# Kernel optimization log

Hardware: AMD Instinct MI355X
Metric: run time of the kernel (lower is better)

## Reference

```python
import jax, jax.numpy as jnp
import numpy as np

B, T, C = 4, 4096, 1024
NEG_INF = -1e38


def setup_inputs() -> dict:
    key = jax.random.key(0)
    ks = jax.random.split(key, 5)
    scale = 0.02  # realistic init scale for CxC projections
    x = jax.random.normal(ks[0], (B, T, C), dtype=jnp.float32)
    key_w = jax.random.normal(ks[1], (C, C), dtype=jnp.float32) * scale
    value_w = jax.random.normal(ks[2], (C, C), dtype=jnp.float32) * scale
    receptance_w = jax.random.normal(ks[3], (C, C), dtype=jnp.float32) * scale
    output_w = jax.random.normal(ks[4], (C, C), dtype=jnp.float32) * scale
    # deterministic param init matching the module's __init__
    time_decay = -5.0 + 8.0 * (jnp.arange(C, dtype=jnp.float32) / (C - 1)) ** 0.7
    time_first = jnp.full((C,), -3.0, dtype=jnp.float32)
    # initial WKV state as in forward() when state is None
    aa0 = jnp.zeros((B, C), dtype=jnp.float32)
    bb0 = jnp.zeros((B, C), dtype=jnp.float32)
    pp0 = jnp.full((B, C), NEG_INF, dtype=jnp.float32)
    return dict(x=x, key_w=key_w, value_w=value_w, receptance_w=receptance_w,
                output_w=output_w, time_decay=time_decay, time_first=time_first,
                aa0=aa0, bb0=bb0, pp0=pp0)


def reference(x, key_w, value_w, receptance_w, output_w,
              time_decay, time_first, aa0, bb0, pp0):
    # projections (torch Linear: y = x @ W.T)
    k = jnp.einsum('btc,dc->btd', x, key_w)        # [B,T,C]
    v = jnp.einsum('btc,dc->btd', x, value_w)      # [B,T,C]
    r = jax.nn.sigmoid(jnp.einsum('btc,dc->btd', x, receptance_w))
    w = jnp.exp(time_decay)  # [C]
    u = time_first           # [C]

    def step(carry, kv):
        aa, bb, pp = carry           # each [B,C]
        kt, vt = kv                  # each [B,C]
        # output at this step (numerically stabilized exp weighting)
        ww = u + kt
        p = jnp.maximum(pp, ww)
        e1 = jnp.exp(pp - p)
        e2 = jnp.exp(ww - p)
        wkv = (e1 * aa + e2 * vt) / (e1 * bb + e2)
        # state update
        ww2 = pp - w
        p2 = jnp.maximum(ww2, kt)
        e1b = jnp.exp(ww2 - p2)
        e2b = jnp.exp(kt - p2)
        return (e1b * aa + e2b * vt, e1b * bb + e2b, p2), wkv

    k_t = jnp.swapaxes(k, 0, 1)  # [T,B,C]
    v_t = jnp.swapaxes(v, 0, 1)
    (aa, bb, pp), wkv = jax.lax.scan(step, (aa0, bb0, pp0), (k_t, v_t))
    wkv = jnp.swapaxes(wkv, 0, 1)  # [B,T,C]

    out = jnp.einsum('btc,dc->btd', r * wkv, output_w)
    return out, aa, bb, pp
```

## Files before the change

kernel.cpp:

```cpp
#include <hip/hip_runtime.h>
#include <stdint.h>

#define BDIM 4
#define TDIM 4096
#define CDIM 1024
#define MDIM (BDIM * TDIM)
#define SSEG 64
#define LSEG 64
#define NCH  (BDIM * CDIM)

typedef __attribute__((ext_vector_type(8))) short bf16x8;
typedef __attribute__((ext_vector_type(4))) float f32x4;

__device__ __forceinline__ unsigned short f2bf(float f) {
    unsigned u = __builtin_bit_cast(unsigned, f);
    u = u + 0x7fffu + ((u >> 16) & 1u);
    return (unsigned short)(u >> 16);
}
__device__ __forceinline__ float bf2f(unsigned short h) {
    unsigned u = ((unsigned)h) << 16;
    return __builtin_bit_cast(float, u);
}

typedef __attribute__((address_space(1))) const unsigned int g_u32;
typedef __attribute__((address_space(3))) unsigned int l_u32;
__device__ __forceinline__ void gload_lds16(const void* g, void* l) {
    __builtin_amdgcn_global_load_lds((g_u32*)g, (l_u32*)l, 16, 0, 0);
}

__global__ void castk(const float* __restrict__ src, unsigned short* __restrict__ dst, int n4) {
    int i = blockIdx.x * blockDim.x + threadIdx.x;
    int stride = gridDim.x * blockDim.x;
    for (int j = i; j < n4; j += stride) {
        float4 f = ((const float4*)src)[j];
        ushort4 o;
        o.x = f2bf(f.x); o.y = f2bf(f.y); o.z = f2bf(f.z); o.w = f2bf(f.w);
        ((ushort4*)dst)[j] = o;
    }
}

template <int MODE>
__global__ __launch_bounds__(256, 2) void gemm_bt(
    const unsigned short* __restrict__ A,
    const unsigned short* __restrict__ Bw,
    void* __restrict__ Y, int K, int N)
{
    __shared__ unsigned short Ash[128 * 32];
    __shared__ unsigned short Bsh[128 * 32];

    const int tid  = threadIdx.x;
    const int wave = tid >> 6;
    const int lane = tid & 63;
    const int row0 = blockIdx.x * 128;
    const int col0 = blockIdx.y * 128;

    const int wm = wave >> 1, wn = wave & 1;
    const int lrow = lane & 15;
    const int lkB  = ((lane >> 4) * 8) * 2;

    f32x4 acc[4][4] = {};

    for (int k0 = 0; k0 < K; k0 += 32) {
#pragma unroll
        for (int j = 0; j < 2; ++j) {
            int chunk = (j * 4 + wave) * 64 + lane;
            int r  = chunk >> 2;
            int c8 = (chunk & 3) * 8;
            const unsigned short* ga = A  + (size_t)(row0 + r) * K + k0 + c8;
            const unsigned short* gb = Bw + (size_t)(col0 + r) * K + k0 + c8;
            gload_lds16(ga, (char*)Ash + chunk * 16);
            gload_lds16(gb, (char*)Bsh + chunk * 16);
        }
        __syncthreads();

        bf16x8 af[4], bfr[4];
#pragma unroll
        for (int mi = 0; mi < 4; ++mi)
            af[mi] = *(const bf16x8*)((const char*)Ash + (wm * 64 + mi * 16 + lrow) * 64 + lkB);
#pragma unroll
        for (int ni = 0; ni < 4; ++ni)
            bfr[ni] = *(const bf16x8*)((const char*)Bsh + (wn * 64 + ni * 16 + lrow) * 64 + lkB);
#pragma unroll
        for (int mi = 0; mi < 4; ++mi)
#pragma unroll
            for (int ni = 0; ni < 4; ++ni)
                acc[mi][ni] = __builtin_amdgcn_mfma_f32_16x16x32_bf16(af[mi], bfr[ni], acc[mi][ni], 0, 0, 0);
        __syncthreads();
    }

    const int crow = (lane >> 4) * 4;
    const int ccol = lane & 15;
#pragma unroll
    for (int mi = 0; mi < 4; ++mi)
#pragma unroll
        for (int ni = 0; ni < 4; ++ni) {
            int gr0 = row0 + wm * 64 + mi * 16 + crow;
            int gc  = col0 + wn * 64 + ni * 16 + ccol;
#pragma unroll
            for (int j = 0; j < 4; ++j) {
                float val = acc[mi][ni][j];
                size_t off = (size_t)(gr0 + j) * N + gc;
                if (MODE == 0) {
                    ((float*)Y)[off] = val;
                } else {
                    float s = 1.0f / (1.0f + __expf(-val));
                    ((unsigned short*)Y)[off] = f2bf(s);
                }
            }
        }
}

__global__ __launch_bounds__(256) void wkv_phase1(
    const float* __restrict__ kf, const float* __restrict__ vf,
    const float* __restrict__ td,
    float* __restrict__ segA, float* __restrict__ segB, float* __restrict__ segP)
{
    const int tid  = blockIdx.x * 256 + threadIdx.x;
    const int lane = tid & 63;
    const int wg   = tid >> 6;
    const int cg   = wg & 63;
    const int s    = wg >> 6;
    const int q    = cg * 64 + lane;
    const int b    = q >> 10;
    const int c    = q & (CDIM - 1);

    const float w = __expf(td[c]);

    float aa = 0.0f, bb = 0.0f, pp = -1e38f;
    size_t idx = (size_t)b * TDIM * CDIM + (size_t)(s * LSEG) * CDIM + c;
#pragma unroll 4
    for (int i = 0; i < LSEG; ++i, idx += CDIM) {
        float kt = kf[idx];
        float vt = vf[idx];
        float ww2 = pp - w;
        float p2  = fmaxf(ww2, kt);
        float e1  = __expf(ww2 - p2);
        float e2  = __expf(kt - p2);
        aa = e1 * aa + e2 * vt;
        bb = e1 * bb + e2;
        pp = p2;
    }
    segA[s * NCH + q] = aa;
    segB[s * NCH + q] = bb;
    segP[s * NCH + q] = pp;
}

__global__ __launch_bounds__(256) void wkv_phase2(
    const float* __restrict__ segA, const float* __restrict__ segB, const float* __restrict__ segP,
    const float* __restrict__ td,
    const float* __restrict__ aa0, const float* __restrict__ bb0, const float* __restrict__ pp0,
    float* __restrict__ preA, float* __restrict__ preB, float* __restrict__ preP,
    float* __restrict__ stout)
{
    const int tid = blockIdx.x * 256 + threadIdx.x;
    const int c = tid & (CDIM - 1);
    const float w  = __expf(td[c]);
    const float Lw = (float)LSEG * w;

    float aa = aa0[tid], bb = bb0[tid], pp = pp0[tid];
    for (int s = 0; s < SSEG; ++s) {
        preA[s * NCH + tid] = aa;
        preB[s * NCH + tid] = bb;
        preP[s * NCH + tid] = pp;
        float al = segA[s * NCH + tid];
        float bl = segB[s * NCH + tid];
        float pl = segP[s * NCH + tid];
        float ppd = pp - Lw;
        float p  = fmaxf(ppd, pl);
        float e1 = __expf(ppd - p);
        float e2 = __expf(pl - p);
        aa = e1 * aa + e2 * al;
        bb = e1 * bb + e2 * bl;
        pp = p;
    }
    stout[tid]            = aa;
    stout[NCH + tid]      = bb;
    stout[2 * NCH + tid]  = pp;
}

__global__ __launch_bounds__(256) void wkv_phase3(
    const float* __restrict__ kf, const float* __restrict__ vf,
    const unsigned short* __restrict__ rb,
    const float* __restrict__ td, const float* __restrict__ tf,
    const float* __restrict__ preA, const float* __restrict__ preB, const float* __restrict__ preP,
    unsigned short* __restrict__ rwkvb)
{
    const int tid  = blockIdx.x * 256 + threadIdx.x;
    const int lane = tid & 63;
    const int wg   = tid >> 6;
    const int cg   = wg & 63;
    const int s    = wg >> 6;
    const int q    = cg * 64 + lane;
    const int b    = q >> 10;
    const int c    = q & (CDIM - 1);

    const float w = __expf(td[c]);
    const float u = tf[c];

    float aa = preA[s * NCH + q];
    float bb = preB[s * NCH + q];
    float pp = preP[s * NCH + q];

    size_t idx = (size_t)b * TDIM * CDIM + (size_t)(s * LSEG) * CDIM + c;
#pragma unroll 4
    for (int i = 0; i < LSEG; ++i, idx += CDIM) {
        float kt = kf[idx];
        float vt = vf[idx];
        float rt = bf2f(rb[idx]);
        float ww = u + kt;
        float p  = fmaxf(pp, ww);
        float e1 = __expf(pp - p);
        float e2 = __expf(ww - p);
        float wkv = (e1 * aa + e2 * vt) / (e1 * bb + e2);
        rwkvb[idx] = f2bf(rt * wkv);
        float ww2 = pp - w;
        float p2  = fmaxf(ww2, kt);
        float e1b = __expf(ww2 - p2);
        float e2b = __expf(kt - p2);
        aa = e1b * aa + e2b * vt;
        bb = e1b * bb + e2b;
        pp = p2;
    }
}

extern "C" void kernel_launch(void* const* d_in, const int* in_sizes, int n_in,
                              void* d_out, int out_size, void* d_ws, size_t ws_size,
                              hipStream_t stream) {
    const float* x   = (const float*)d_in[0];
    const float* kw  = (const float*)d_in[1];
    const float* vw  = (const float*)d_in[2];
    const float* rw  = (const float*)d_in[3];
    const float* ow  = (const float*)d_in[4];
    const float* td  = (const float*)d_in[5];
    const float* tf  = (const float*)d_in[6];
    const float* aa0 = (const float*)d_in[7];
    const float* bb0 = (const float*)d_in[8];
    const float* pp0 = (const float*)d_in[9];
    float* out = (float*)d_out;

    char* ws = (char*)d_ws;
    unsigned short* xb    = (unsigned short*)(ws);
    unsigned short* kwb   = (unsigned short*)(ws + 33554432);
    unsigned short* vwb   = (unsigned short*)(ws + 35651584);
    unsigned short* rwb   = (unsigned short*)(ws + 37748736);
    unsigned short* owb   = (unsigned short*)(ws + 39845888);
    float*          kfb   = (float*)(ws + 41943040);
    float*          vfb   = (float*)(ws + 109051904);
    unsigned short* rbb   = (unsigned short*)(ws + 176160768);
    unsigned short* rwkvb = (unsigned short*)(ws + 209715200);
    float* segA = (float*)(ws + 0);
    float* segB = (float*)(ws + 1048576);
    float* segP = (float*)(ws + 2097152);
    float* preA = (float*)(ws + 3145728);
    float* preB = (float*)(ws + 4194304);
    float* preP = (float*)(ws + 5242880);

    castk<<<2048, 256, 0, stream>>>(x,  xb,  MDIM * CDIM / 4);
    castk<<<512,  256, 0, stream>>>(kw, kwb, CDIM * CDIM / 4);
    castk<<<512,  256, 0, stream>>>(vw, vwb, CDIM * CDIM / 4);
    castk<<<512,  256, 0, stream>>>(rw, rwb, CDIM * CDIM / 4);
    castk<<<512,  256, 0, stream>>>(ow, owb, CDIM * CDIM / 4);

    dim3 gg(MDIM / 128, CDIM / 128);
    gemm_bt<0><<<gg, 256, 0, stream>>>(xb, kwb, kfb, CDIM, CDIM);
    gemm_bt<0><<<gg, 256, 0, stream>>>(xb, vwb, vfb, CDIM, CDIM);
    gemm_bt<1><<<gg, 256, 0, stream>>>(xb, rwb, rbb, CDIM, CDIM);

    wkv_phase1<<<NCH * SSEG / 256, 256, 0, stream>>>(kfb, vfb, td, segA, segB, segP);
    wkv_phase2<<<NCH / 256, 256, 0, stream>>>(segA, segB, segP, td, aa0, bb0, pp0,
                                              preA, preB, preP, out + (size_t)MDIM * CDIM);
    wkv_phase3<<<NCH * SSEG / 256, 256, 0, stream>>>(kfb, vfb, rbb, td, tf,
                                                     preA, preB, preP, rwkvb);

    gemm_bt<0><<<gg, 256, 0, stream>>>(rwkvb, owb, out, CDIM, CDIM);
}
```

Before: 267.1 us.

## Fuse K/V/R projections into one 256x256 pipelined GEMM with bf16 outputs

Replaces the 128x128 GEMM with a 256x256-tile, 512-thread kernel. It uses double-buffered, XOR-swizzled LDS staging, interleaved MFMA and load phases with setprio, and XCD-aware block remapping. The K, V and R projections now run as a single launch over a concatenated weight matrix. K and V are stored as bf16 instead of fp32, which halves the bytes the WKV phases read and write. The risks are lower precision in k and v feeding the exp-based recurrence, and the large 128KB LDS footprint per block limiting occupancy.

```diff
diff --git a/kernel.cpp b/kernel.cpp
--- a/kernel.cpp
+++ b/kernel.cpp
@@ -8,6 +8,11 @@
 #define SSEG 64
 #define LSEG 64
 #define NCH  (BDIM * CDIM)
+
+#define GK   1024
+#define GK2  2048
+#define NTK  16
+#define NT4  64
 
 typedef __attribute__((ext_vector_type(8))) short bf16x8;
 typedef __attribute__((ext_vector_type(4))) float f32x4;
@@ -40,78 +45,176 @@
 }
 
 template <int MODE>
-__global__ __launch_bounds__(256, 2) void gemm_bt(
+__global__ __launch_bounds__(512, 2) void gemm256(
     const unsigned short* __restrict__ A,
     const unsigned short* __restrict__ Bw,
-    void* __restrict__ Y, int K, int N)
+    unsigned short* __restrict__ oK, unsigned short* __restrict__ oV,
+    unsigned short* __restrict__ oR, float* __restrict__ oF)
 {
-    __shared__ unsigned short Ash[128 * 32];
-    __shared__ unsigned short Bsh[128 * 32];
+    extern __shared__ char sh[];
+    char* shA = sh;
+    char* shB = sh + 65536;
 
     const int tid  = threadIdx.x;
     const int wave = tid >> 6;
     const int lane = tid & 63;
-    const int row0 = blockIdx.x * 128;
-    const int col0 = blockIdx.y * 128;
-
-    const int wm = wave >> 1, wn = wave & 1;
+    const int wm   = wave >> 2;
+    const int wn   = wave & 3;
     const int lrow = lane & 15;
-    const int lkB  = ((lane >> 4) * 8) * 2;
-
-    f32x4 acc[4][4] = {};
-
-    for (int k0 = 0; k0 < K; k0 += 32) {
+    const int koct = lane >> 4;
+
+    const int nwg = gridDim.x;
+    const int cpx = nwg >> 3;
+    const int bid = blockIdx.x;
+    const int wg  = (bid & 7) * cpx + (bid >> 3);
+    const int mt  = wg & 63;
+    const int nt  = wg >> 6;
+    const size_t row0 = (size_t)mt * 256;
+    const size_t col0 = (size_t)nt * 256;
+
+    const char* gA = (const char*)A  + row0 * GK2;
+    const char* gB = (const char*)Bw + col0 * GK2;
+
+    auto stage_half = [&](int h) {
+        if (h >= NT4) return;
+        int t = h >> 2, part = h & 3, slot = t & 1;
+        int isA = part >> 1, half = part & 1;
+        const char* gbase = isA ? gA : gB;
+        char* lbase = (isA ? shA : shB) + (slot * 2 + half) * 16384;
 #pragma unroll
         for (int j = 0; j < 2; ++j) {
-            int chunk = (j * 4 + wave) * 64 + lane;
-            int r  = chunk >> 2;
-            int c8 = (chunk & 3) * 8;
-            const unsigned short* ga = A  + (size_t)(row0 + r) * K + k0 + c8;
-            const unsigned short* gb = Bw + (size_t)(col0 + r) * K + k0 + c8;
-            gload_lds16(ga, (char*)Ash + chunk * 16);
-            gload_lds16(gb, (char*)Bsh + chunk * 16);
+            int d = (j * 512 + tid) * 16;
+            int r = d >> 7;
+            int cb = (d & 127) ^ ((r & 7) << 4);
+            gload_lds16(gbase + (size_t)(half * 128 + r) * GK2 + t * 128 + cb, lbase + d);
         }
-        __syncthreads();
-
-        bf16x8 af[4], bfr[4];
-#pragma unroll
-        for (int mi = 0; mi < 4; ++mi)
-            af[mi] = *(const bf16x8*)((const char*)Ash + (wm * 64 + mi * 16 + lrow) * 64 + lkB);
-#pragma unroll
-        for (int ni = 0; ni < 4; ++ni)
-            bfr[ni] = *(const bf16x8*)((const char*)Bsh + (wn * 64 + ni * 16 + lrow) * 64 + lkB);
-#pragma unroll
-        for (int mi = 0; mi < 4; ++mi)
-#pragma unroll
-            for (int ni = 0; ni < 4; ++ni)
-                acc[mi][ni] = __builtin_amdgcn_mfma_f32_16x16x32_bf16(af[mi], bfr[ni], acc[mi][ni], 0, 0, 0);
-        __syncthreads();
+    };
+
+#pragma unroll
+    for (int h = 0; h < 7; ++h) stage_half(h);
+    asm volatile("s_waitcnt vmcnt(6)" ::: "memory");
+    asm volatile("s_barrier" ::: "memory");
+
+    f32x4 acc[8][4] = {};
+    bf16x8 afr[8][2], bfr[4][2];
+
+    for (int t = 0; t < NTK; ++t) {
+        const int slot = t & 1;
+        const int aoff = (slot * 2 + wm) * 16384;
+        const int boff = (slot * 2 + (wn >> 1)) * 16384;
+        const int brb  = (wn & 1) * 64;
+
+#pragma unroll
+        for (int mi = 0; mi < 4; ++mi) {
+            int r = mi * 16 + lrow, sw = (r & 7) << 4;
+#pragma unroll
+            for (int ks = 0; ks < 2; ++ks)
+                afr[mi][ks] = *(const bf16x8*)(shA + aoff + r * 128 + ((ks * 64 + koct * 16) ^ sw));
+        }
+#pragma unroll
+        for (int ni = 0; ni < 4; ++ni) {
+            int r = brb + ni * 16 + lrow, sw = (r & 7) << 4;
+#pragma unroll
+            for (int ks = 0; ks < 2; ++ks)
+                bfr[ni][ks] = *(const bf16x8*)(shB + boff + r * 128 + ((ks * 64 + koct * 16) ^ sw));
+        }
+        stage_half(4 * t + 7);
+        asm volatile("s_barrier" ::: "memory");
+        __builtin_amdgcn_s_setprio(1);
+#pragma unroll
+        for (int a = 0; a < 4; ++a)
+#pragma unroll
+            for (int b = 0; b < 2; ++b)
+#pragma unroll
+                for (int ks = 0; ks < 2; ++ks)
+                    acc[a][b] = __builtin_amdgcn_mfma_f32_16x16x32_bf16(afr[a][ks], bfr[b][ks], acc[a][b], 0, 0, 0);
+        __builtin_amdgcn_s_setprio(0);
+        asm volatile("s_barrier" ::: "memory");
+
+#pragma unroll
+        for (int mi = 4; mi < 8; ++mi) {
+            int r = mi * 16 + lrow, sw = (r & 7) << 4;
+#pragma unroll
+            for (int ks = 0; ks < 2; ++ks)
+                afr[mi][ks] = *(const bf16x8*)(shA + aoff + r * 128 + ((ks * 64 + koct * 16) ^ sw));
+        }
+        stage_half(4 * t + 8);
+        asm volatile("s_barrier" ::: "memory");
+        __builtin_amdgcn_s_setprio(1);
+#pragma unroll
+        for (int a = 0; a < 4; ++a)
+#pragma unroll
+            for (int b = 0; b < 2; ++b)
+#pragma unroll
+                for (int ks = 0; ks < 2; ++ks)
+                    acc[a][2 + b] = __builtin_amdgcn_mfma_f32_16x16x32_bf16(afr[a][ks], bfr[2 + b][ks], acc[a][2 + b], 0, 0, 0);
+        __builtin_amdgcn_s_setprio(0);
+        asm volatile("s_barrier" ::: "memory");
+
+        stage_half(4 * t + 9);
+        asm volatile("s_barrier" ::: "memory");
+        __builtin_amdgcn_s_setprio(1);
+#pragma unroll
+        for (int a = 0; a < 4; ++a)
+#pragma unroll
+            for (int b = 0; b < 2; ++b)
+#pragma unroll
+                for (int ks = 0; ks < 2; ++ks)
+                    acc[4 + a][b] = __builtin_amdgcn_mfma_f32_16x16x32_bf16(afr[4 + a][ks], bfr[b][ks], acc[4 + a][b], 0, 0, 0);
+        __builtin_amdgcn_s_setprio(0);
+        asm volatile("s_barrier" ::: "memory");
+
+        stage_half(4 * t + 10);
+        asm volatile("s_barrier" ::: "memory");
+        __builtin_amdgcn_s_setprio(1);
+#pragma unroll
+        for (int a = 0; a < 4; ++a)
+#pragma unroll
+            for (int b = 0; b < 2; ++b)
+#pragma unroll
+                for (int ks = 0; ks < 2; ++ks)
+                    acc[4 + a][2 + b] = __builtin_amdgcn_mfma_f32_16x16x32_bf16(afr[4 + a][ks], bfr[2 + b][ks], acc[4 + a][2 + b], 0, 0, 0);
+        __builtin_amdgcn_s_setprio(0);
+        if (t < NTK - 2)       asm volatile("s_waitcnt vmcnt(6)" ::: "memory");
+        else if (t == NTK - 2) asm volatile("s_waitcnt vmcnt(0)" ::: "memory");
+        asm volatile("s_barrier" ::: "memory");
     }
 
     const int crow = (lane >> 4) * 4;
     const int ccol = lane & 15;
-#pragma unroll
-    for (int mi = 0; mi < 4; ++mi)
-#pragma unroll
-        for (int ni = 0; ni < 4; ++ni) {
-            int gr0 = row0 + wm * 64 + mi * 16 + crow;
-            int gc  = col0 + wn * 64 + ni * 16 + ccol;
-#pragma unroll
-            for (int j = 0; j < 4; ++j) {
-                float val = acc[mi][ni][j];
-                size_t off = (size_t)(gr0 + j) * N + gc;
-                if (MODE == 0) {
-                    ((float*)Y)[off] = val;
-                } else {
-                    float s = 1.0f / (1.0f + __expf(-val));
-                    ((unsigned short*)Y)[off] = f2bf(s);
+    if (MODE == 1) {
+#pragma unroll
+        for (int mi = 0; mi < 8; ++mi)
+#pragma unroll
+            for (int ni = 0; ni < 4; ++ni) {
+                size_t gr = row0 + wm * 128 + mi * 16 + crow;
+                size_t gc = col0 + wn * 64 + ni * 16 + ccol;
+#pragma unroll
+                for (int j = 0; j < 4; ++j)
+                    oF[(gr + j) * 1024 + gc] = acc[mi][ni][j];
+            }
+    } else {
+        const int region = nt >> 2;
+        unsigned short* dst = (region == 0) ? oK : ((region == 1) ? oV : oR);
+        const size_t cb0 = (size_t)(nt & 3) * 256;
+#pragma unroll
+        for (int mi = 0; mi < 8; ++mi)
+#pragma unroll
+            for (int ni = 0; ni < 4; ++ni) {
+                size_t gr = row0 + wm * 128 + mi * 16 + crow;
+                size_t gc = cb0 + wn * 64 + ni * 16 + ccol;
+#pragma unroll
+                for (int j = 0; j < 4; ++j) {
+                    float val = acc[mi][ni][j];
+                    if (region == 2) val = 1.0f / (1.0f + __expf(-val));
+                    dst[(gr + j) * 1024 + gc] = f2bf(val);
                 }
             }
-        }
+    }
 }
 
 __global__ __launch_bounds__(256) void wkv_phase1(
-    const float* __restrict__ kf, const float* __restrict__ vf,
+    const unsigned short* __restrict__ kf, const unsigned short* __restrict__ vf,
     const float* __restrict__ td,
     float* __restrict__ segA, float* __restrict__ segB, float* __restrict__ segP)
 {
@@ -130,8 +233,8 @@
     size_t idx = (size_t)b * TDIM * CDIM + (size_t)(s * LSEG) * CDIM + c;
 #pragma unroll 4
     for (int i = 0; i < LSEG; ++i, idx += CDIM) {
-        float kt = kf[idx];
-        float vt = vf[idx];
+        float kt = bf2f(kf[idx]);
+        float vt = bf2f(vf[idx]);
         float ww2 = pp - w;
         float p2  = fmaxf(ww2, kt);
         float e1  = __expf(ww2 - p2);
@@ -173,13 +276,13 @@
         bb = e1 * bb + e2 * bl;
         pp = p;
     }
-    stout[tid]            = aa;
-    stout[NCH + tid]      = bb;
-    stout[2 * NCH + tid]  = pp;
+    stout[tid]           = aa;
+    stout[NCH + tid]     = bb;
+    stout[2 * NCH + tid] = pp;
 }
 
 __global__ __launch_bounds__(256) void wkv_phase3(
-    const float* __restrict__ kf, const float* __restrict__ vf,
+    const unsigned short* __restrict__ kf, const unsigned short* __restrict__ vf,
     const unsigned short* __restrict__ rb,
     const float* __restrict__ td, const float* __restrict__ tf,
     const float* __restrict__ preA, const float* __restrict__ preB, const float* __restrict__ preP,
@@ -204,8 +307,8 @@
     size_t idx = (size_t)b * TDIM * CDIM + (size_t)(s * LSEG) * CDIM + c;
 #pragma unroll 4
     for (int i = 0; i < LSEG; ++i, idx += CDIM) {
-        float kt = kf[idx];
-        float vt = vf[idx];
+        float kt = bf2f(kf[idx]);
+        float vt = bf2f(vf[idx]);
         float rt = bf2f(rb[idx]);
         float ww = u + kt;
         float p  = fmaxf(pp, ww);
@@ -239,32 +342,30 @@
     float* out = (float*)d_out;
 
     char* ws = (char*)d_ws;
-    unsigned short* xb    = (unsigned short*)(ws);
-    unsigned short* kwb   = (unsigned short*)(ws + 33554432);
-    unsigned short* vwb   = (unsigned short*)(ws + 35651584);
-    unsigned short* rwb   = (unsigned short*)(ws + 37748736);
-    unsigned short* owb   = (unsigned short*)(ws + 39845888);
-    float*          kfb   = (float*)(ws + 41943040);
-    float*          vfb   = (float*)(ws + 109051904);
-    unsigned short* rbb   = (unsigned short*)(ws + 176160768);
-    unsigned short* rwkvb = (unsigned short*)(ws + 209715200);
-    float* segA = (float*)(ws + 0);
-    float* segB = (float*)(ws + 1048576);
-    float* segP = (float*)(ws + 2097152);
-    float* preA = (float*)(ws + 3145728);
-    float* preB = (float*)(ws + 4194304);
-    float* preP = (float*)(ws + 5242880);
-
-    castk<<<2048, 256, 0, stream>>>(x,  xb,  MDIM * CDIM / 4);
-    castk<<<512,  256, 0, stream>>>(kw, kwb, CDIM * CDIM / 4);
-    castk<<<512,  256, 0, stream>>>(vw, vwb, CDIM * CDIM / 4);
-    castk<<<512,  256, 0, stream>>>(rw, rwb, CDIM * CDIM / 4);
-    castk<<<512,  256, 0, stream>>>(ow, owb, CDIM * CDIM / 4);
-
-    dim3 gg(MDIM / 128, CDIM / 128);
-    gemm_bt<0><<<gg, 256, 0, stream>>>(xb, kwb, kfb, CDIM, CDIM);
-    gemm_bt<0><<<gg, 256, 0, stream>>>(xb, vwb, vfb, CDIM, CDIM);
-    gemm_bt<1><<<gg, 256, 0, stream>>>(xb, rwb, rbb, CDIM, CDIM);
+    unsigned short* wf    = (unsigned short*)(ws);
+    unsigned short* owb   = (unsigned short*)(ws + 6291456);
+    unsigned short* xb    = (unsigned short*)(ws + 8388608);
+    unsigned short* kfb   = (unsigned short*)(ws + 41943040);
+    unsigned short* vfb   = (unsigned short*)(ws + 75497472);
+    unsigned short* rbb   = (unsigned short*)(ws + 109051904);
+    unsigned short* rwkvb = (unsigned short*)(ws + 142606336);
+    float* segA = (float*)(ws + 176160768);
+    float* segB = (float*)(ws + 177209344);
+    float* segP = (float*)(ws + 178257920);
+    float* preA = (float*)(ws + 179306496);
+    float* preB = (float*)(ws + 180355072);
+    float* preP = (float*)(ws + 181403648);
+
+    hipFuncSetAttribute((const void*)gemm256<0>, hipFuncAttributeMaxDynamicSharedMemorySize, 131072);
+    hipFuncSetAttribute((const void*)gemm256<1>, hipFuncAttributeMaxDynamicSharedMemorySize, 131072);
+
+    castk<<<2048, 256, 0, stream>>>(x,  xb, MDIM * CDIM / 4);
+    castk<<<512,  256, 0, stream>>>(kw, wf,            CDIM * CDIM / 4);
+    castk<<<512,  256, 0, stream>>>(vw, wf + 1048576,  CDIM * CDIM / 4);
+    castk<<<512,  256, 0, stream>>>(rw, wf + 2097152,  CDIM * CDIM / 4);
+    castk<<<512,  256, 0, stream>>>(ow, owb,           CDIM * CDIM / 4);
+
+    gemm256<0><<<768, 512, 131072, stream>>>(xb, wf, kfb, vfb, rbb, nullptr);
 
     wkv_phase1<<<NCH * SSEG / 256, 256, 0, stream>>>(kfb, vfb, td, segA, segB, segP);
     wkv_phase2<<<NCH / 256, 256, 0, stream>>>(segA, segB, segP, td, aa0, bb0, pp0,
@@ -272,5 +373,5 @@
     wkv_phase3<<<NCH * SSEG / 256, 256, 0, stream>>>(kfb, vfb, rbb, td, tf,
                                                      preA, preB, preP, rwkvb);
 
-    gemm_bt<0><<<gg, 256, 0, stream>>>(rwkvb, owb, out, CDIM, CDIM);
-}
+    gemm256<1><<<256, 512, 131072, stream>>>(rwkvb, owb, nullptr, nullptr, nullptr, out);
+}
```

New measurement: 245.8 us. 8.0% less time.
